# Optimization experiments

Hardware: AMD Instinct MI355X
Metric: run time of the kernel (lower is better)

Reference implementation:

```python
import jax, jax.numpy as jnp
import numpy as np

HIDDEN = 2048
NUM_HEADS = 16
KEY_DIM = 1024      # hidden * expand_k (0.5)
VALUE_DIM = 2048    # hidden * expand_v (1.0)
HEAD_K = KEY_DIM // NUM_HEADS   # 64
HEAD_V = VALUE_DIM // NUM_HEADS # 128
EPS = 1e-5
B, T = 8, 4096


def _rmsnorm(x, w, eps=EPS):
    var = jnp.mean(jnp.square(x), axis=-1, keepdims=True)
    return x * jax.lax.rsqrt(var + eps) * w


def setup_inputs() -> dict:
    key = jax.random.key(0)
    ks = jax.random.split(key, 7)
    s = 1.0 / np.sqrt(HIDDEN)
    return {
        "hidden_states": jax.random.normal(ks[0], (B, T, HIDDEN), dtype=jnp.float32),
        "recurrent_state": jax.random.normal(ks[1], (B, NUM_HEADS, HEAD_K, HEAD_V), dtype=jnp.float32),
        "norm_w": jnp.ones((HIDDEN,), dtype=jnp.float32),
        "q_w": jax.random.uniform(ks[2], (KEY_DIM, HIDDEN), jnp.float32, -s, s),
        "v_norm_w": jnp.ones((HEAD_V,), dtype=jnp.float32),
        "o_w": jax.random.uniform(ks[3], (HIDDEN, VALUE_DIM), jnp.float32, -s, s),
        "gate_w": jax.random.uniform(ks[4], (HIDDEN, HIDDEN), jnp.float32, -s, s),
    }


def reference(hidden_states, recurrent_state, norm_w, q_w, v_norm_w, o_w, gate_w):
    x = _rmsnorm(hidden_states, norm_w)                       # (B,T,D)
    q = x @ q_w.T                                             # (B,T,KEY_DIM)
    q = q.reshape(*q.shape[:2], NUM_HEADS, HEAD_K)            # (B,T,H,K)
    # L2 normalize along last dim (F.normalize default eps=1e-12 on the norm)
    norm = jnp.maximum(jnp.linalg.norm(q, axis=-1, keepdims=True), 1e-12)
    q = q / norm
    o = jnp.einsum('bthk,bhkv->bthv', q, recurrent_state)     # (B,T,H,V)
    o = _rmsnorm(o, v_norm_w)
    o = o.reshape(*o.shape[:2], VALUE_DIM)                    # (B,T,VALUE_DIM)
    o = o @ o_w.T                                             # (B,T,D)
    gate = jax.nn.sigmoid(x @ gate_w.T)                       # (B,T,D)
    return gate * o
```

## Files before the change

### kernel.cpp

```cpp
#include <hip/hip_runtime.h>

typedef unsigned short u16;
typedef unsigned int u32;
typedef __attribute__((ext_vector_type(4))) float f32x4;
typedef __attribute__((ext_vector_type(8))) short short8;
typedef __attribute__((ext_vector_type(4))) short short4v;

#define HIDDEN 2048
#define NHEADS 16
#define KEYDIM 1024
#define VALDIM 2048
#define HEADK 64
#define HEADV 128
#define NBATCH 8
#define SEQ 4096
#define NTOK (NBATCH * SEQ)

__device__ __forceinline__ u16 f2bf(float f) {
  union { float f; u32 u; } c; c.f = f;
  u32 r = c.u + 0x7FFFu + ((c.u >> 16) & 1u);
  return (u16)(r >> 16);
}
__device__ __forceinline__ float bf2f(u16 h) {
  union { u32 u; float f; } c; c.u = ((u32)h) << 16;
  return c.f;
}

__global__ __launch_bounds__(256) void cast_bf16_k(const float* __restrict__ in,
                                                   u16* __restrict__ out, int n4) {
  int i = blockIdx.x * blockDim.x + threadIdx.x;
  if (i >= n4) return;
  f32x4 v = *(const f32x4*)(in + (size_t)i * 4);
  short4v o;
  o[0] = (short)f2bf(v[0]); o[1] = (short)f2bf(v[1]);
  o[2] = (short)f2bf(v[2]); o[3] = (short)f2bf(v[3]);
  *(short4v*)(out + (size_t)i * 4) = o;
}

__global__ __launch_bounds__(256) void rmsnorm_cast_k(const float* __restrict__ x,
                                                      const float* __restrict__ w,
                                                      u16* __restrict__ xb) {
  int r = blockIdx.x;
  int tid = threadIdx.x;
  const float* xp = x + (size_t)r * HIDDEN + tid * 8;
  f32x4 v0 = *(const f32x4*)xp;
  f32x4 v1 = *(const f32x4*)(xp + 4);
  float ss = v0[0]*v0[0]+v0[1]*v0[1]+v0[2]*v0[2]+v0[3]*v0[3]
           + v1[0]*v1[0]+v1[1]*v1[1]+v1[2]*v1[2]+v1[3]*v1[3];
  #pragma unroll
  for (int m = 32; m >= 1; m >>= 1) ss += __shfl_xor(ss, m);
  __shared__ float red[4];
  if ((tid & 63) == 0) red[tid >> 6] = ss;
  __syncthreads();
  float tot = red[0] + red[1] + red[2] + red[3];
  float inv = rsqrtf(tot * (1.0f / HIDDEN) + 1e-5f);
  const float* wp = w + tid * 8;
  f32x4 w0 = *(const f32x4*)wp;
  f32x4 w1 = *(const f32x4*)(wp + 4);
  short8 o;
  o[0] = (short)f2bf(v0[0] * inv * w0[0]);
  o[1] = (short)f2bf(v0[1] * inv * w0[1]);
  o[2] = (short)f2bf(v0[2] * inv * w0[2]);
  o[3] = (short)f2bf(v0[3] * inv * w0[3]);
  o[4] = (short)f2bf(v1[0] * inv * w1[0]);
  o[5] = (short)f2bf(v1[1] * inv * w1[1]);
  o[6] = (short)f2bf(v1[2] * inv * w1[2]);
  o[7] = (short)f2bf(v1[3] * inv * w1[3]);
  *(short8*)(xb + (size_t)r * HIDDEN + tid * 8) = o;
}


__device__ __forceinline__ void gload16(const u16* g, u16* l) {
  __builtin_amdgcn_global_load_lds((const __attribute__((address_space(1))) void*)g,
                                   (__attribute__((address_space(3))) void*)l, 16, 0, 0);
}

#define BAR()                                  \
  do {                                         \
    __builtin_amdgcn_s_barrier();              \
    __builtin_amdgcn_sched_barrier(0x0F);      \
  } while (0)

template <int MODE>
__global__ __launch_bounds__(512, 2) void gemm4r_k(const u16* __restrict__ A,
                                                   const u16* __restrict__ Bw,
                                                   void* __restrict__ Cptr,
                                                   int M, int N, int K) {
  extern __shared__ u16 lds[];
  const int tid = threadIdx.x;
  const int wid = tid >> 6;
  const int wm = wid >> 2;
  const int wn = wid & 3;
  const int l = tid & 63;
  const int lr = l & 15;
  const int kq = l >> 4;

  const int ntn = N >> 8;
  const int per = gridDim.x >> 3;
  const int b = blockIdx.x;
  const int sidx = (b & 7) * per + (b >> 3);
  const int mt = sidx / ntn;
  const int nt = sidx - mt * ntn;

  const u16* Ag = A + (size_t)(mt * 256) * K;
  const u16* Bg = Bw + (size_t)(nt * 256) * K;

  const int srow = tid >> 2;
  const int kel = (((tid & 3) ^ ((tid >> 3) & 3)) << 3);

#define STAGE_A(c)                                               \
  do {                                                           \
    const u16* _s = Ag + (size_t)srow * K + ((c) << 5) + kel;    \
    u16* _d = lds + (((c) & 3) << 14) + tid * 8;                 \
    gload16(_s, _d);                                             \
    gload16(_s + (size_t)128 * K, _d + 4096);                    \
  } while (0)
#define STAGE_B(c)                                               \
  do {                                                           \
    const u16* _s = Bg + (size_t)srow * K + ((c) << 5) + kel;    \
    u16* _d = lds + (((c) & 3) << 14) + 8192 + tid * 8;          \
    gload16(_s, _d);                                             \
    gload16(_s + (size_t)128 * K, _d + 4096);                    \
  } while (0)

  int aoff[2][4], boff[4];
  #pragma unroll
  for (int mi = 0; mi < 4; ++mi) {
    int R0 = wm * 128 + mi * 16 + lr;
    aoff[0][mi] = R0 * 32 + ((kq ^ ((R0 >> 1) & 3)) << 3);
    int R1 = R0 + 64;
    aoff[1][mi] = R1 * 32 + ((kq ^ ((R1 >> 1) & 3)) << 3);
  }
  #pragma unroll
  for (int n = 0; n < 4; ++n) {
    int R = wn * 64 + n * 16 + lr;
    boff[n] = 8192 + R * 32 + ((kq ^ ((R >> 1) & 3)) << 3);
  }

  short8 afr[4], bfr[4];
  f32x4 acc[8][4] = {};

  STAGE_A(0); STAGE_B(0);
  STAGE_A(1); STAGE_B(1);
  STAGE_A(2); STAGE_B(2);
  asm volatile("s_waitcnt vmcnt(8)" ::: "memory");
  BAR();

  const int NT = K >> 5;
  #pragma unroll 1
  for (int c = 0; c < NT; ++c) {
    const u16* bufT = lds + ((c & 3) << 14);
    const int g3 = (c + 3 < NT);

    #pragma unroll
    for (int n = 0; n < 4; ++n) bfr[n] = *(const short8*)(bufT + boff[n]);
    #pragma unroll
    for (int mi = 0; mi < 4; ++mi) afr[mi] = *(const short8*)(bufT + aoff[0][mi]);
    if (g3) STAGE_A(c + 3);
    BAR();
    __builtin_amdgcn_s_setprio(1);
    #pragma unroll
    for (int mi = 0; mi < 4; ++mi) {
      #pragma unroll
      for (int n = 0; n < 4; ++n)
        acc[mi][n] = __builtin_amdgcn_mfma_f32_16x16x32_bf16(afr[mi], bfr[n], acc[mi][n], 0, 0, 0);
    }
    __builtin_amdgcn_s_setprio(0);
    BAR();

    #pragma unroll
    for (int mi = 0; mi < 4; ++mi) afr[mi] = *(const short8*)(bufT + aoff[1][mi]);
    if (g3) STAGE_B(c + 3);
    BAR();
    __builtin_amdgcn_s_setprio(1);
    #pragma unroll
    for (int mi = 0; mi < 4; ++mi) {
      #pragma unroll
      for (int n = 0; n < 4; ++n)
        acc[4 + mi][n] = __builtin_amdgcn_mfma_f32_16x16x32_bf16(afr[mi], bfr[n], acc[4 + mi][n], 0, 0, 0);
    }
    __builtin_amdgcn_s_setprio(0);
    if (g3)               asm volatile("s_waitcnt vmcnt(8)" ::: "memory");
    else if (c + 2 < NT)  asm volatile("s_waitcnt vmcnt(4)" ::: "memory");
    else if (c + 1 < NT)  asm volatile("s_waitcnt vmcnt(0)" ::: "memory");
    BAR();
  }
#undef STAGE_A
#undef STAGE_B

  const int rowB = mt * 256 + wm * 128 + kq * 4;
  const int colB = nt * 256 + wn * 64 + lr;
  #pragma unroll
  for (int m = 0; m < 8; ++m) {
    #pragma unroll
    for (int n = 0; n < 4; ++n) {
      #pragma unroll
      for (int j = 0; j < 4; ++j) {
        int row = rowB + m * 16 + j;
        int col = colB + n * 16;
        size_t idx = (size_t)row * N + col;
        float v = acc[m][n][j];
        if constexpr (MODE == 0) {
          ((u16*)Cptr)[idx] = f2bf(v);
        } else if constexpr (MODE == 1) {
          ((float*)Cptr)[idx] = 1.0f / (1.0f + __expf(-v));
        } else {
          float* O = (float*)Cptr;
          O[idx] = O[idx] * v;
        }
      }
    }
  }
}

__global__ __launch_bounds__(256) void glaread_k(const u16* __restrict__ q,
                                                 const float* __restrict__ S,
                                                 const float* __restrict__ vw,
                                                 u16* __restrict__ omid) {
  int bh = blockIdx.x;
  int b = bh >> 4, h = bh & 15;
  int tid = threadIdx.x;
  int w = tid >> 6, l = tid & 63;
  int lr = l & 15, kq = l >> 4;

  const float* Sp = S + (size_t)bh * HEADK * HEADV;
  short8 bfrag[8][2];
  #pragma unroll
  for (int n = 0; n < 8; ++n) {
    #pragma unroll
    for (int s = 0; s < 2; ++s) {
      #pragma unroll
      for (int i = 0; i < 8; ++i)
        bfrag[n][s][i] =
            (short)f2bf(Sp[(size_t)(s * 32 + kq * 8 + i) * HEADV + n * 16 + lr]);
    }
  }
  float vwn[8];
  #pragma unroll
  for (int n = 0; n < 8; ++n) vwn[n] = vw[n * 16 + lr];

  #pragma unroll 1
  for (int it = 0; it < 8; ++it) {
    int t0 = blockIdx.y * 512 + it * 64 + w * 16;
    const u16* qp = q + (size_t)(b * SEQ + t0 + lr) * KEYDIM + h * HEADK;
    short8 a0 = *(const short8*)(qp + kq * 8);
    short8 a1 = *(const short8*)(qp + 32 + kq * 8);

    float ss = 0.f;
    #pragma unroll
    for (int i = 0; i < 8; ++i) {
      float x0 = bf2f((u16)a0[i]), x1 = bf2f((u16)a1[i]);
      ss += x0 * x0 + x1 * x1;
    }
    ss += __shfl_xor(ss, 16);
    ss += __shfl_xor(ss, 32);
    float sc = 1.0f / fmaxf(sqrtf(ss), 1e-12f);

    short8 an0, an1;
    #pragma unroll
    for (int i = 0; i < 8; ++i) {
      an0[i] = (short)f2bf(bf2f((u16)a0[i]) * sc);
      an1[i] = (short)f2bf(bf2f((u16)a1[i]) * sc);
    }

    f32x4 acc[8] = {};
    #pragma unroll
    for (int n = 0; n < 8; ++n) {
      acc[n] = __builtin_amdgcn_mfma_f32_16x16x32_bf16(an0, bfrag[n][0], acc[n], 0, 0, 0);
      acc[n] = __builtin_amdgcn_mfma_f32_16x16x32_bf16(an1, bfrag[n][1], acc[n], 0, 0, 0);
    }

    float part[4] = {0.f, 0.f, 0.f, 0.f};
    #pragma unroll
    for (int n = 0; n < 8; ++n) {
      #pragma unroll
      for (int j = 0; j < 4; ++j) part[j] += acc[n][j] * acc[n][j];
    }
    #pragma unroll
    for (int msk = 1; msk <= 8; msk <<= 1) {
      #pragma unroll
      for (int j = 0; j < 4; ++j) part[j] += __shfl_xor(part[j], msk);
    }
    #pragma unroll
    for (int j = 0; j < 4; ++j) {
      float inv = rsqrtf(part[j] * (1.0f / HEADV) + 1e-5f);
      int tok = t0 + kq * 4 + j;
      u16* op = omid + (size_t)(b * SEQ + tok) * VALDIM + h * HEADV;
      #pragma unroll
      for (int n = 0; n < 8; ++n)
        op[n * 16 + lr] = f2bf(acc[n][j] * inv * vwn[n]);
    }
  }
}

extern "C" void kernel_launch(void* const* d_in, const int* in_sizes, int n_in,
                              void* d_out, int out_size, void* d_ws, size_t ws_size,
                              hipStream_t stream) {
  const float* hs = (const float*)d_in[0];
  const float* S  = (const float*)d_in[1];
  const float* nw = (const float*)d_in[2];
  const float* qw = (const float*)d_in[3];
  const float* vw = (const float*)d_in[4];
  const float* ow = (const float*)d_in[5];
  const float* gw = (const float*)d_in[6];
  float* out = (float*)d_out;

  u16* xb   = (u16*)d_ws;
  u16* q    = xb + (size_t)NTOK * HIDDEN;
  u16* qwb  = q + (size_t)NTOK * KEYDIM;
  u16* owb  = qwb + (size_t)KEYDIM * HIDDEN;
  u16* gwb  = owb + (size_t)HIDDEN * VALDIM;
  u16* omid = xb;

  const size_t LDSB = 131072;

  cast_bf16_k<<<(KEYDIM * HIDDEN / 4 + 255) / 256, 256, 0, stream>>>(qw, qwb, KEYDIM * HIDDEN / 4);
  cast_bf16_k<<<(HIDDEN * VALDIM / 4 + 255) / 256, 256, 0, stream>>>(ow, owb, HIDDEN * VALDIM / 4);
  cast_bf16_k<<<(HIDDEN * HIDDEN / 4 + 255) / 256, 256, 0, stream>>>(gw, gwb, HIDDEN * HIDDEN / 4);

  rmsnorm_cast_k<<<NTOK, 256, 0, stream>>>(hs, nw, xb);

  gemm4r_k<0><<<dim3((NTOK / 256) * (KEYDIM / 256)), 512, LDSB, stream>>>(xb, qwb, q, NTOK, KEYDIM, HIDDEN);

  gemm4r_k<1><<<dim3((NTOK / 256) * (HIDDEN / 256)), 512, LDSB, stream>>>(xb, gwb, out, NTOK, HIDDEN, HIDDEN);

  glaread_k<<<dim3(NBATCH * NHEADS, SEQ / 512), 256, 0, stream>>>(q, S, vw, omid);

  gemm4r_k<2><<<dim3((NTOK / 256) * (HIDDEN / 256)), 512, LDSB, stream>>>(omid, owb, out, NTOK, HIDDEN, VALDIM);
}
```

Baseline: 1.010 ms.

## Restructure GEMM pipeline to K=64 half-stage prefetch and stash gate in bf16

The GEMM main loop now handles 64-wide K steps as two 32-wide half-slots in a 4-slot ring. It prefetches only one step ahead and interleaves A and B staging between MFMA halves, with a new LDS swizzle and plain compiler barriers in place of sched_barrier. When the workspace is large enough, the gate GEMM writes a bf16 sigmoid buffer instead of fp32 output, and the final GEMM multiplies by it instead of read-modify-writing fp32 out. This is meant to cut barrier overhead and fp32 gate traffic, at the cost of a shallower prefetch and an extra workspace requirement.

Result: faster. 898.7 us (-11.0%).

```diff
diff --git a/kernel.cpp b/kernel.cpp
--- a/kernel.cpp
+++ b/kernel.cpp
@@ -77,14 +77,16 @@
 
 #define BAR()                                  \
   do {                                         \
+    asm volatile("" ::: "memory");             \
     __builtin_amdgcn_s_barrier();              \
-    __builtin_amdgcn_sched_barrier(0x0F);      \
+    asm volatile("" ::: "memory");             \
   } while (0)
 
 template <int MODE>
-__global__ __launch_bounds__(512, 2) void gemm4r_k(const u16* __restrict__ A,
+__global__ __launch_bounds__(512, 2) void gemmkh_k(const u16* __restrict__ A,
                                                    const u16* __restrict__ Bw,
                                                    void* __restrict__ Cptr,
+                                                   const u16* __restrict__ Gate,
                                                    int M, int N, int K) {
   extern __shared__ u16 lds[];
   const int tid = threadIdx.x;
@@ -106,87 +108,98 @@
   const u16* Bg = Bw + (size_t)(nt * 256) * K;
 
   const int srow = tid >> 2;
-  const int kel = (((tid & 3) ^ ((tid >> 3) & 3)) << 3);
-
-#define STAGE_A(c)                                               \
-  do {                                                           \
-    const u16* _s = Ag + (size_t)srow * K + ((c) << 5) + kel;    \
-    u16* _d = lds + (((c) & 3) << 14) + tid * 8;                 \
-    gload16(_s, _d);                                             \
-    gload16(_s + (size_t)128 * K, _d + 4096);                    \
+  const int kel32 = (((tid & 3) ^ ((tid >> 2) & 3)) << 3);
+
+#define SLOTB(c, kk) ((((2 * (c)) + (kk)) & 3) * 16384)
+#define STAGE_AH(c, kk)                                                        \
+  do {                                                                         \
+    const u16* _s = Ag + (size_t)srow * K + ((c) << 6) + ((kk) << 5) + kel32;  \
+    u16* _d = lds + SLOTB(c, kk) + tid * 8;                                    \
+    gload16(_s, _d);                                                           \
+    gload16(_s + (size_t)128 * K, _d + 4096);                                  \
   } while (0)
-#define STAGE_B(c)                                               \
-  do {                                                           \
-    const u16* _s = Bg + (size_t)srow * K + ((c) << 5) + kel;    \
-    u16* _d = lds + (((c) & 3) << 14) + 8192 + tid * 8;          \
-    gload16(_s, _d);                                             \
-    gload16(_s + (size_t)128 * K, _d + 4096);                    \
+#define STAGE_BH(c, kk)                                                        \
+  do {                                                                         \
+    const u16* _s = Bg + (size_t)srow * K + ((c) << 6) + ((kk) << 5) + kel32;  \
+    u16* _d = lds + SLOTB(c, kk) + 8192 + tid * 8;                             \
+    gload16(_s, _d);                                                           \
+    gload16(_s + (size_t)128 * K, _d + 4096);                                  \
   } while (0)
 
   int aoff[2][4], boff[4];
   #pragma unroll
-  for (int mi = 0; mi < 4; ++mi) {
-    int R0 = wm * 128 + mi * 16 + lr;
-    aoff[0][mi] = R0 * 32 + ((kq ^ ((R0 >> 1) & 3)) << 3);
-    int R1 = R0 + 64;
-    aoff[1][mi] = R1 * 32 + ((kq ^ ((R1 >> 1) & 3)) << 3);
+  for (int mh = 0; mh < 2; ++mh) {
+    #pragma unroll
+    for (int mi = 0; mi < 4; ++mi) {
+      int R = wm * 128 + mh * 64 + mi * 16 + lr;
+      aoff[mh][mi] = R * 32 + ((kq ^ (R & 3)) << 3);
+    }
   }
   #pragma unroll
   for (int n = 0; n < 4; ++n) {
     int R = wn * 64 + n * 16 + lr;
-    boff[n] = 8192 + R * 32 + ((kq ^ ((R >> 1) & 3)) << 3);
+    boff[n] = 8192 + R * 32 + ((kq ^ (R & 3)) << 3);
   }
 
   short8 afr[4], bfr[4];
   f32x4 acc[8][4] = {};
 
-  STAGE_A(0); STAGE_B(0);
-  STAGE_A(1); STAGE_B(1);
-  STAGE_A(2); STAGE_B(2);
-  asm volatile("s_waitcnt vmcnt(8)" ::: "memory");
+  auto LDA = [&](int slot, int mh) {
+    const u16* p = lds + slot * 16384;
+    #pragma unroll
+    for (int mi = 0; mi < 4; ++mi) afr[mi] = *(const short8*)(p + aoff[mh][mi]);
+  };
+  auto LDB = [&](int slot) {
+    const u16* p = lds + slot * 16384;
+    #pragma unroll
+    for (int n = 0; n < 4; ++n) bfr[n] = *(const short8*)(p + boff[n]);
+  };
+  auto MMA = [&](int mh) {
+    __builtin_amdgcn_s_setprio(1);
+    #pragma unroll
+    for (int mi = 0; mi < 4; ++mi) {
+      #pragma unroll
+      for (int n = 0; n < 4; ++n)
+        acc[mh * 4 + mi][n] =
+            __builtin_amdgcn_mfma_f32_16x16x32_bf16(afr[mi], bfr[n], acc[mh * 4 + mi][n], 0, 0, 0);
+    }
+    __builtin_amdgcn_s_setprio(0);
+  };
+
+  STAGE_AH(0, 0); STAGE_BH(0, 0);
+  STAGE_AH(0, 1); STAGE_BH(0, 1);
+  asm volatile("s_waitcnt vmcnt(4)" ::: "memory");
   BAR();
 
-  const int NT = K >> 5;
+  const int NT = K >> 6;
   #pragma unroll 1
   for (int c = 0; c < NT; ++c) {
-    const u16* bufT = lds + ((c & 3) << 14);
-    const int g3 = (c + 3 < NT);
-
-    #pragma unroll
-    for (int n = 0; n < 4; ++n) bfr[n] = *(const short8*)(bufT + boff[n]);
-    #pragma unroll
-    for (int mi = 0; mi < 4; ++mi) afr[mi] = *(const short8*)(bufT + aoff[0][mi]);
-    if (g3) STAGE_A(c + 3);
+    const int g = (c + 1 < NT);
+    const int s0 = (2 * c) & 3, s1 = (2 * c + 1) & 3;
+
+    LDA(s0, 0); LDB(s0);
     BAR();
-    __builtin_amdgcn_s_setprio(1);
-    #pragma unroll
-    for (int mi = 0; mi < 4; ++mi) {
-      #pragma unroll
-      for (int n = 0; n < 4; ++n)
-        acc[mi][n] = __builtin_amdgcn_mfma_f32_16x16x32_bf16(afr[mi], bfr[n], acc[mi][n], 0, 0, 0);
-    }
-    __builtin_amdgcn_s_setprio(0);
+    if (g) STAGE_AH(c + 1, 0);
+    MMA(0);
+    LDA(s0, 1);
+    if (g) asm volatile("s_waitcnt vmcnt(2)" ::: "memory");
+    else   asm volatile("s_waitcnt vmcnt(0)" ::: "memory");
     BAR();
-
-    #pragma unroll
-    for (int mi = 0; mi < 4; ++mi) afr[mi] = *(const short8*)(bufT + aoff[1][mi]);
-    if (g3) STAGE_B(c + 3);
+    if (g) STAGE_BH(c + 1, 0);
+    MMA(1);
+    LDA(s1, 0); LDB(s1);
     BAR();
-    __builtin_amdgcn_s_setprio(1);
-    #pragma unroll
-    for (int mi = 0; mi < 4; ++mi) {
-      #pragma unroll
-      for (int n = 0; n < 4; ++n)
-        acc[4 + mi][n] = __builtin_amdgcn_mfma_f32_16x16x32_bf16(afr[mi], bfr[n], acc[4 + mi][n], 0, 0, 0);
-    }
-    __builtin_amdgcn_s_setprio(0);
-    if (g3)               asm volatile("s_waitcnt vmcnt(8)" ::: "memory");
-    else if (c + 2 < NT)  asm volatile("s_waitcnt vmcnt(4)" ::: "memory");
-    else if (c + 1 < NT)  asm volatile("s_waitcnt vmcnt(0)" ::: "memory");
+    if (g) STAGE_AH(c + 1, 1);
+    MMA(0);
+    LDA(s1, 1);
+    if (g) asm volatile("s_waitcnt vmcnt(2)" ::: "memory");
     BAR();
-  }
-#undef STAGE_A
-#undef STAGE_B
+    if (g) STAGE_BH(c + 1, 1);
+    MMA(1);
+  }
+#undef STAGE_AH
+#undef STAGE_BH
+#undef SLOTB
 
   const int rowB = mt * 256 + wm * 128 + kq * 4;
   const int colB = nt * 256 + wn * 64 + lr;
@@ -203,6 +216,10 @@
         if constexpr (MODE == 0) {
           ((u16*)Cptr)[idx] = f2bf(v);
         } else if constexpr (MODE == 1) {
+          ((u16*)Cptr)[idx] = f2bf(1.0f / (1.0f + __expf(-v)));
+        } else if constexpr (MODE == 2) {
+          ((float*)Cptr)[idx] = v * bf2f(Gate[idx]);
+        } else if constexpr (MODE == 3) {
           ((float*)Cptr)[idx] = 1.0f / (1.0f + __expf(-v));
         } else {
           float* O = (float*)Cptr;
@@ -310,7 +327,12 @@
   u16* qwb  = q + (size_t)NTOK * KEYDIM;
   u16* owb  = qwb + (size_t)KEYDIM * HIDDEN;
   u16* gwb  = owb + (size_t)HIDDEN * VALDIM;
+  u16* gatebuf = gwb + (size_t)HIDDEN * HIDDEN;
   u16* omid = xb;
+
+  const size_t need = ((size_t)NTOK * HIDDEN * 2) * 2 + (size_t)NTOK * KEYDIM * 2 +
+                      ((size_t)KEYDIM * HIDDEN + 2 * (size_t)HIDDEN * HIDDEN) * 2;
+  const bool bigws = ws_size >= need;
 
   const size_t LDSB = 131072;
 
@@ -320,11 +342,19 @@
 
   rmsnorm_cast_k<<<NTOK, 256, 0, stream>>>(hs, nw, xb);
 
-  gemm4r_k<0><<<dim3((NTOK / 256) * (KEYDIM / 256)), 512, LDSB, stream>>>(xb, qwb, q, NTOK, KEYDIM, HIDDEN);
-
-  gemm4r_k<1><<<dim3((NTOK / 256) * (HIDDEN / 256)), 512, LDSB, stream>>>(xb, gwb, out, NTOK, HIDDEN, HIDDEN);
+  gemmkh_k<0><<<dim3((NTOK / 256) * (KEYDIM / 256)), 512, LDSB, stream>>>(xb, qwb, q, nullptr, NTOK, KEYDIM, HIDDEN);
+
+  if (bigws) {
+    gemmkh_k<1><<<dim3((NTOK / 256) * (HIDDEN / 256)), 512, LDSB, stream>>>(xb, gwb, gatebuf, nullptr, NTOK, HIDDEN, HIDDEN);
+  } else {
+    gemmkh_k<3><<<dim3((NTOK / 256) * (HIDDEN / 256)), 512, LDSB, stream>>>(xb, gwb, out, nullptr, NTOK, HIDDEN, HIDDEN);
+  }
 
   glaread_k<<<dim3(NBATCH * NHEADS, SEQ / 512), 256, 0, stream>>>(q, S, vw, omid);
 
-  gemm4r_k<2><<<dim3((NTOK / 256) * (HIDDEN / 256)), 512, LDSB, stream>>>(omid, owb, out, NTOK, HIDDEN, VALDIM);
-}
+  if (bigws) {
+    gemmkh_k<2><<<dim3((NTOK / 256) * (HIDDEN / 256)), 512, LDSB, stream>>>(omid, owb, out, gatebuf, NTOK, HIDDEN, VALDIM);
+  } else {
+    gemmkh_k<4><<<dim3((NTOK / 256) * (HIDDEN / 256)), 512, LDSB, stream>>>(omid, owb, out, nullptr, NTOK, HIDDEN, VALDIM);
+  }
+}
```
